# Optimization experiments

Measured on AMD Instinct MI355X. Metric: run time of the kernel, lower is better.

## Reference

```python
import jax, jax.numpy as jnp
import numpy as np

N_HEAD = 16


def setup_inputs() -> dict:
    key = jax.random.key(0)
    ks = jax.random.split(key, 6)
    B, T, H = 4, 2048, 1024
    inp = jax.random.normal(ks[0], (B, T, H), dtype=jnp.float32)
    # padding mask: valid prefix of random length in [T//2, T] per batch row
    lengths = jax.random.randint(ks[1], (B, 1), T // 2, T + 1)
    mask = jnp.arange(T)[None, :] < lengths  # (B, T) bool
    s = 0.02
    w_qkv = jax.random.normal(ks[2], (H, 3 * H), dtype=jnp.float32) * s
    b_qkv = jax.random.normal(ks[3], (3 * H,), dtype=jnp.float32) * s
    w_out = jax.random.normal(ks[4], (H, H), dtype=jnp.float32) * s
    b_out = jax.random.normal(ks[5], (H,), dtype=jnp.float32) * s
    return {"input": inp, "mask": mask, "w_qkv": w_qkv, "b_qkv": b_qkv,
            "w_out": w_out, "b_out": b_out}


def reference(input, mask, w_qkv, b_qkv, w_out, b_out):
    B, T, H = input.shape
    hd = H // N_HEAD
    qkv = input @ w_qkv + b_qkv                       # (B, T, 3H)
    q, k, v = jnp.split(qkv, 3, axis=-1)
    # (B, T, H) -> (B, nh, T, hd)
    q = q.reshape(B, T, N_HEAD, hd).transpose(0, 2, 1, 3)
    k = k.reshape(B, T, N_HEAD, hd).transpose(0, 2, 1, 3)
    v = v.reshape(B, T, N_HEAD, hd).transpose(0, 2, 1, 3)
    scores = jnp.einsum('bhqd,bhkd->bhqk', q, k) / jnp.sqrt(jnp.float32(hd))
    causal = jnp.tril(jnp.ones((T, T), dtype=bool))   # (T, T)
    full_mask = causal[None, None, :, :] & mask[:, None, None, :]  # (B,1,T,T) bcast over heads
    scores = jnp.where(full_mask, scores, -jnp.inf)
    attn = jax.nn.softmax(scores, axis=-1)            # (B, nh, T, T)
    o = jnp.einsum('bhqk,bhkd->bhqd', attn, v)        # (B, nh, T, hd)
    o = o.transpose(0, 2, 1, 3).reshape(B, T, H)
    return o @ w_out + b_out
```

## Files before the change

### kernel.cpp

```cpp
#include <hip/hip_runtime.h>
#include <math.h>

#define B_  4
#define T_  2048
#define H_  1024
#define NH  16
#define HD  64
#define H3  3072

typedef short bf16x8 __attribute__((ext_vector_type(8)));
typedef short bf16x4 __attribute__((ext_vector_type(4)));
typedef float f32x4  __attribute__((ext_vector_type(4)));

#define SC2F 0.18033688011112042f

__device__ __forceinline__ unsigned short f2bf(float f) {
    union { float f; unsigned u; } v; v.f = f;
    unsigned u = v.u;
    unsigned r = (u + 0x7fffu + ((u >> 16) & 1u)) >> 16;
    return (unsigned short)r;
}

__device__ __forceinline__ void gload_lds16(const void* g, void* l) {
    __builtin_amdgcn_global_load_lds(
        (const __attribute__((address_space(1))) unsigned*)g,
        (__attribute__((address_space(3))) unsigned*)l, 16, 0, 0);
}

__device__ __forceinline__ f32x4 mfma_16x16x16_bf16(bf16x4 a, bf16x4 b, f32x4 c) {
#if __has_builtin(__builtin_amdgcn_mfma_f32_16x16x16_bf16)
    return __builtin_amdgcn_mfma_f32_16x16x16_bf16(a, b, c, 0, 0, 0);
#elif __has_builtin(__builtin_amdgcn_mfma_f32_16x16x16bf16_1k)
    return __builtin_amdgcn_mfma_f32_16x16x16bf16_1k(a, b, c, 0, 0, 0);
#else
    f32x4 d;
    asm volatile("v_mfma_f32_16x16x16_bf16 %0, %1, %2, %3"
                 : "=v"(d) : "v"(a), "v"(b), "v"(c));
    return d;
#endif
}

__global__ void lengths_kernel(const void* mask, int* lengths) {
    int b = blockIdx.x;
    int t = threadIdx.x;
    const unsigned* mu = (const unsigned*)mask;
    bool is_byte = (mu[0] == 0x01010101u);
    int cnt = 0;
    if (is_byte) {
        const unsigned char* m8 = (const unsigned char*)mask;
        for (int i = t; i < T_; i += 256) cnt += (m8[b * T_ + i] != 0);
    } else {
        const unsigned* m32 = (const unsigned*)mask;
        for (int i = t; i < T_; i += 256) cnt += (m32[b * T_ + i] != 0);
    }
    __shared__ int red[256];
    red[t] = cnt;
    __syncthreads();
    for (int s = 128; s > 0; s >>= 1) {
        if (t < s) red[t] += red[t + s];
        __syncthreads();
    }
    if (t == 0) lengths[b] = red[0];
}

__global__ void convert_bf16_kernel(const float* __restrict__ x,
                                    unsigned short* __restrict__ y, int n) {
    int i = (blockIdx.x * 256 + threadIdx.x) * 4;
    if (i < n) {
        float4 v = *(const float4*)(x + i);
        ushort4 o;
        o.x = f2bf(v.x); o.y = f2bf(v.y); o.z = f2bf(v.z); o.w = f2bf(v.w);
        *(ushort4*)(y + i) = o;
    }
}

__global__ void transpose_bf16_kernel(const float* __restrict__ in,
                                      unsigned short* __restrict__ out,
                                      int K, int N) {
    __shared__ unsigned short tile[32][33];
    int kb = blockIdx.y * 32, nb = blockIdx.x * 32;
    int tx = threadIdx.x, ty = threadIdx.y;
    for (int i = 0; i < 32; i += 8)
        tile[ty + i][tx] = f2bf(in[(long)(kb + ty + i) * N + nb + tx]);
    __syncthreads();
    for (int i = 0; i < 32; i += 8)
        out[(long)(nb + ty + i) * K + kb + tx] = tile[tx][ty + i];
}

template <bool BF16_OUT, bool KSCALE, bool VSPLIT>
__global__ __launch_bounds__(256) void gemm_kernel(
    const unsigned short* __restrict__ A,
    const unsigned short* __restrict__ Bt,
    const float* __restrict__ bias,
    void* __restrict__ C,
    unsigned short* __restrict__ Vt,
    int M, int N, int K)
{
    __shared__ unsigned short Asm[128][32];
    __shared__ unsigned short Bsm[128][32];

    int tn = blockIdx.x * 128, tm = blockIdx.y * 128;
    int tid = threadIdx.x;
    int wid = tid >> 6, lane = tid & 63, quad = lane >> 4, lr = lane & 15;
    int wm = (wid & 1) * 64, wn = (wid >> 1) * 64;
    int grow = lane >> 2, gcol = (lane & 3) * 8;

    f32x4 acc[4][4] = {};

    for (int k0 = 0; k0 < K; k0 += 32) {
        __syncthreads();
#pragma unroll
        for (int t = 0; t < 2; t++) {
            int ar = wid * 32 + t * 16 + grow;
            gload_lds16(A  + (long)(tm + ar) * K + k0 + gcol, &Asm[wid * 32 + t * 16][0]);
            gload_lds16(Bt + (long)(tn + ar) * K + k0 + gcol, &Bsm[wid * 32 + t * 16][0]);
        }
        __syncthreads();

        bf16x8 af[4], bfv[4];
#pragma unroll
        for (int i = 0; i < 4; i++) af[i]  = *(const bf16x8*)(&Asm[wm + i * 16 + lr][quad * 8]);
#pragma unroll
        for (int j = 0; j < 4; j++) bfv[j] = *(const bf16x8*)(&Bsm[wn + j * 16 + lr][quad * 8]);
#pragma unroll
        for (int i = 0; i < 4; i++)
#pragma unroll
            for (int j = 0; j < 4; j++)
                acc[i][j] = __builtin_amdgcn_mfma_f32_16x16x32_bf16(af[i], bfv[j], acc[i][j], 0, 0, 0);
    }

    if (VSPLIT && tn >= 2 * H_) {
#pragma unroll
        for (int i = 0; i < 4; i++)
#pragma unroll
            for (int j = 0; j < 4; j++) {
                int col = tn + wn + j * 16 + lr;
                float bs = bias[col];
                int feat = col - 2 * H_;
                int tok0 = tm + wm + i * 16 + quad * 4;
                int bb = tok0 >> 11;
                unsigned d0 = (unsigned)f2bf(acc[i][j][0] + bs) |
                              ((unsigned)f2bf(acc[i][j][1] + bs) << 16);
                unsigned d1 = (unsigned)f2bf(acc[i][j][2] + bs) |
                              ((unsigned)f2bf(acc[i][j][3] + bs) << 16);
                unsigned short* dst = Vt + ((long)(bb * 1024 + feat)) * T_ + (tok0 & (T_ - 1));
                *(uint2*)dst = make_uint2(d0, d1);
            }
        return;
    }

#pragma unroll
    for (int i = 0; i < 4; i++)
#pragma unroll
        for (int j = 0; j < 4; j++) {
            int col = tn + wn + j * 16 + lr;
            float bs = bias[col];
            bool ks = KSCALE && (col >= H_) && (col < 2 * H_);
#pragma unroll
            for (int r = 0; r < 4; r++) {
                int row = tm + wm + i * 16 + quad * 4 + r;
                float v = acc[i][j][r] + bs;
                if (ks) v *= SC2F;
                if (BF16_OUT)
                    ((unsigned short*)C)[(long)row * N + col] = f2bf(v);
                else
                    ((float*)C)[(long)row * N + col] = v;
            }
        }
}

__global__ __launch_bounds__(256) void attn_kernel(
    const unsigned short* __restrict__ QKV,
    const unsigned short* __restrict__ Vt,
    const int* __restrict__ lengths,
    unsigned short* __restrict__ O)
{
    int idx = blockIdx.x;
    int bh = idx & 63;
    int pr = idx >> 6;
    int b = bh >> 4, h = bh & 15;
    int len = lengths[b];

    int tid = threadIdx.x;
    int wid = tid >> 6, lane = tid & 63, quad = lane >> 4, lr = lane & 15;

    __shared__ unsigned short Qs[128][72];
    __shared__ unsigned short Kd[2][64][72];
    __shared__ unsigned short Vd[2][64][72];

    const long qkv_base = (long)b * T_ * H3;
    int srow = tid >> 2, scb = (tid & 3) * 16;
    const unsigned short* kbase = QKV + qkv_base + (long)srow * H3 + H_ + h * HD + scb;
    const unsigned short* vbase = Vt + ((long)(bh * 64 + srow)) * T_ + scb;

    for (int pass = 0; pass < 2; pass++) {
        int qt = pass ? pr : (15 - pr);
        int q0 = qt * 128;

        __syncthreads();
        {
            int row = tid >> 1, cb = (tid & 1) * 32;
            const unsigned short* src = QKV + qkv_base + (long)(q0 + row) * H3 + h * HD + cb;
#pragma unroll
            for (int i = 0; i < 4; i++)
                *(float4*)(&Qs[row][cb + i * 8]) = *(const float4*)(src + i * 8);
        }
        {
            float4 k0 = *(const float4*)(kbase);
            float4 k1 = *(const float4*)(kbase + 8);
            float4 v0 = *(const float4*)(vbase);
            float4 v1 = *(const float4*)(vbase + 8);
            *(float4*)(&Kd[0][srow][scb])     = k0;
            *(float4*)(&Kd[0][srow][scb + 8]) = k1;
            *(float4*)(&Vd[0][srow][scb])     = v0;
            *(float4*)(&Vd[0][srow][scb + 8]) = v1;
        }
        __syncthreads();

        bf16x8 qf[2][2];
#pragma unroll
        for (int nq = 0; nq < 2; nq++)
#pragma unroll
            for (int ks = 0; ks < 2; ks++)
                qf[nq][ks] = *(const bf16x8*)(&Qs[wid * 32 + nq * 16 + lr][ks * 32 + quad * 8]);

        float l_i[2] = { 0.f, 0.f };
        f32x4 Oacc[4][2] = {};

        int kmax = min(q0 + 127, len - 1);
        int n_kt = (kmax >> 6) + 1;
        int q_wave_lo = q0 + wid * 32;
        int q_wave_hi = q_wave_lo + 31;
        int myq[2] = { q_wave_lo + lr, q_wave_lo + 16 + lr };

        const unsigned short* kp = kbase + (long)64 * H3;
        const unsigned short* vp = vbase + 64;

        for (int kt = 0; kt < n_kt; kt++) {
            int cur = kt & 1;
            float4 pk0, pk1, pv0, pv1;
            bool pf = (kt + 1 < n_kt);
            if (pf) {
                pk0 = *(const float4*)(kp);
                pk1 = *(const float4*)(kp + 8);
                pv0 = *(const float4*)(vp);
                pv1 = *(const float4*)(vp + 8);
                kp += (long)64 * H3;
                vp += 64;
            }

            int k_lo = kt * 64;
            if (!(k_lo > q_wave_hi || k_lo >= len)) {
                f32x4 Sacc[4][2] = {};
#pragma unroll
                for (int ks = 0; ks < 2; ks++) {
#pragma unroll
                    for (int mt = 0; mt < 4; mt++) {
                        bf16x8 kf = *(const bf16x8*)(&Kd[cur][mt * 16 + lr][ks * 32 + quad * 8]);
                        Sacc[mt][0] = __builtin_amdgcn_mfma_f32_16x16x32_bf16(kf, qf[0][ks], Sacc[mt][0], 0, 0, 0);
                        Sacc[mt][1] = __builtin_amdgcn_mfma_f32_16x16x32_bf16(kf, qf[1][ks], Sacc[mt][1], 0, 0, 0);
                    }
                }

                bool full = (k_lo + 63 <= q_wave_lo) && (k_lo + 63 < len);
                float rs[2] = { 0.f, 0.f };
                unsigned pkk[4][2][2];
#pragma unroll
                for (int mt = 0; mt < 4; mt++)
#pragma unroll
                    for (int nq = 0; nq < 2; nq++) {
                        float p[4];
#pragma unroll
                        for (int r = 0; r < 4; r++) {
                            float s = Sacc[mt][nq][r];
                            if (!full) {
                                int key = k_lo + mt * 16 + quad * 4 + r;
                                bool ok = (key <= myq[nq]) && (key < len);
                                s = ok ? s : -INFINITY;
                            }
                            p[r] = __builtin_amdgcn_exp2f(s);
                            rs[nq] += p[r];
                        }
                        pkk[mt][nq][0] = __builtin_amdgcn_perm(__float_as_uint(p[1]), __float_as_uint(p[0]), 0x07060302);
                        pkk[mt][nq][1] = __builtin_amdgcn_perm(__float_as_uint(p[3]), __float_as_uint(p[2]), 0x07060302);
                    }

#pragma unroll
                for (int nq = 0; nq < 2; nq++) {
                    float v = rs[nq];
                    v += __shfl_xor(v, 16);
                    v += __shfl_xor(v, 32);
                    l_i[nq] += v;
                }

#pragma unroll
                for (int mt = 0; mt < 4; mt++) {
                    union { unsigned u[2]; bf16x4 v; } bu[2];
                    bu[0].u[0] = pkk[mt][0][0]; bu[0].u[1] = pkk[mt][0][1];
                    bu[1].u[0] = pkk[mt][1][0]; bu[1].u[1] = pkk[mt][1][1];
#pragma unroll
                    for (int md = 0; md < 4; md++) {
                        bf16x4 vf = *(const bf16x4*)(&Vd[cur][md * 16 + lr][mt * 16 + quad * 4]);
                        Oacc[md][0] = mfma_16x16x16_bf16(vf, bu[0].v, Oacc[md][0]);
                        Oacc[md][1] = mfma_16x16x16_bf16(vf, bu[1].v, Oacc[md][1]);
                    }
                }
            }

            if (pf) {
                *(float4*)(&Kd[cur ^ 1][srow][scb])     = pk0;
                *(float4*)(&Kd[cur ^ 1][srow][scb + 8]) = pk1;
                *(float4*)(&Vd[cur ^ 1][srow][scb])     = pv0;
                *(float4*)(&Vd[cur ^ 1][srow][scb + 8]) = pv1;
            }
            __syncthreads();
        }

        {
            float inv[2] = { 1.f / l_i[0], 1.f / l_i[1] };
#pragma unroll
            for (int nq = 0; nq < 2; nq++)
#pragma unroll
                for (int md = 0; md < 4; md++)
#pragma unroll
                    for (int rp = 0; rp < 2; rp++) {
                        float e0 = Oacc[md][nq][rp * 2]     * inv[nq];
                        float e1 = Oacc[md][nq][rp * 2 + 1] * inv[nq];
                        unsigned w = __builtin_amdgcn_perm(__float_as_uint(e1), __float_as_uint(e0), 0x07060302);
                        *(unsigned*)(&Qs[wid * 32 + nq * 16 + lr][md * 16 + quad * 4 + rp * 2]) = w;
                    }
            __asm__ volatile("s_waitcnt lgkmcnt(0)" ::: "memory");
            int row = lane >> 1, cb = (lane & 1) * 32;
            long tok = (long)b * T_ + q0 + wid * 32 + row;
#pragma unroll
            for (int i = 0; i < 4; i++) {
                float4 v = *(const float4*)(&Qs[wid * 32 + row][cb + i * 8]);
                *(float4*)(&O[tok * H_ + h * HD + cb + i * 8]) = v;
            }
        }
    }
}

extern "C" void kernel_launch(void* const* d_in, const int* in_sizes, int n_in,
                              void* d_out, int out_size, void* d_ws, size_t ws_size,
                              hipStream_t stream) {
    const float* X    = (const float*)d_in[0];
    const void*  mask = d_in[1];
    const float* Wqkv = (const float*)d_in[2];
    const float* bqkv = (const float*)d_in[3];
    const float* Wout = (const float*)d_in[4];
    const float* bout = (const float*)d_in[5];

    char* ws = (char*)d_ws;
    int* lengths          = (int*)ws;
    unsigned short* WqkvT = (unsigned short*)(ws + 256);
    unsigned short* WoutT = WqkvT + (long)H3 * H_;
    unsigned short* QKV   = WoutT + (long)H_ * H_;
    unsigned short* Xbf   = QKV + (long)B_ * T_ * H3;
    unsigned short* Vt    = Xbf + (long)B_ * T_ * H_;
    unsigned short* Obf   = Xbf;

    const int M = B_ * T_;

    lengths_kernel<<<B_, 256, 0, stream>>>(mask, lengths);
    convert_bf16_kernel<<<(M * H_ / 4 + 255) / 256, 256, 0, stream>>>(X, Xbf, M * H_);
    transpose_bf16_kernel<<<dim3(H3 / 32, H_ / 32), dim3(32, 8), 0, stream>>>(Wqkv, WqkvT, H_, H3);
    transpose_bf16_kernel<<<dim3(H_ / 32, H_ / 32), dim3(32, 8), 0, stream>>>(Wout, WoutT, H_, H_);
    gemm_kernel<true, true, true><<<dim3(H3 / 128, M / 128), 256, 0, stream>>>(
        Xbf, WqkvT, bqkv, QKV, Vt, M, H3, H_);
    attn_kernel<<<B_ * NH * 8, 256, 0, stream>>>(QKV, Vt, lengths, Obf);
    gemm_kernel<false, false, false><<<dim3(H_ / 128, M / 128), 256, 0, stream>>>(
        Obf, WoutT, bout, d_out, nullptr, M, H_, H_);
}
```

Measured before the change: 300.0 us.

## Use 32x32 MFMA with swizzled LDS in GEMM, one q-tile per attention block

```diff
diff --git a/kernel.cpp b/kernel.cpp
--- a/kernel.cpp
+++ b/kernel.cpp
@@ -11,6 +11,7 @@
 typedef short bf16x8 __attribute__((ext_vector_type(8)));
 typedef short bf16x4 __attribute__((ext_vector_type(4)));
 typedef float f32x4  __attribute__((ext_vector_type(4)));
+typedef float f32x16 __attribute__((ext_vector_type(16)));
 
 #define SC2F 0.18033688011112042f
 
@@ -74,11 +75,18 @@
     }
 }
 
-__global__ void transpose_bf16_kernel(const float* __restrict__ in,
-                                      unsigned short* __restrict__ out,
-                                      int K, int N) {
+__global__ void transpose2_kernel(const float* __restrict__ Wqkv,
+                                  unsigned short* __restrict__ WqkvT,
+                                  const float* __restrict__ Wout,
+                                  unsigned short* __restrict__ WoutT) {
     __shared__ unsigned short tile[32][33];
-    int kb = blockIdx.y * 32, nb = blockIdx.x * 32;
+    const int K = H_;
+    const float* in;
+    unsigned short* out;
+    int N, nb;
+    if (blockIdx.x < 96) { in = Wqkv; out = WqkvT; N = H3; nb = blockIdx.x * 32; }
+    else                 { in = Wout; out = WoutT; N = H_; nb = (blockIdx.x - 96) * 32; }
+    int kb = blockIdx.y * 32;
     int tx = threadIdx.x, ty = threadIdx.y;
     for (int i = 0; i < 32; i += 8)
         tile[ty + i][tx] = f2bf(in[(long)(kb + ty + i) * N + nb + tx]);
@@ -101,11 +109,14 @@
 
     int tn = blockIdx.x * 128, tm = blockIdx.y * 128;
     int tid = threadIdx.x;
-    int wid = tid >> 6, lane = tid & 63, quad = lane >> 4, lr = lane & 15;
+    int wid = tid >> 6, lane = tid & 63;
+    int l31 = lane & 31, lh = lane >> 5;
     int wm = (wid & 1) * 64, wn = (wid >> 1) * 64;
-    int grow = lane >> 2, gcol = (lane & 3) * 8;
-
-    f32x4 acc[4][4] = {};
+    int grow = lane >> 2;
+    int gcol = (((lane & 3) ^ (grow & 3) ^ ((grow >> 2) & 3))) * 8;
+    int rkey = (l31 & 3) ^ ((l31 >> 2) & 3);
+
+    f32x16 acc[2][2] = {};
 
     for (int k0 = 0; k0 < K; k0 += 32) {
         __syncthreads();
@@ -117,50 +128,60 @@
         }
         __syncthreads();
 
-        bf16x8 af[4], bfv[4];
-#pragma unroll
-        for (int i = 0; i < 4; i++) af[i]  = *(const bf16x8*)(&Asm[wm + i * 16 + lr][quad * 8]);
-#pragma unroll
-        for (int j = 0; j < 4; j++) bfv[j] = *(const bf16x8*)(&Bsm[wn + j * 16 + lr][quad * 8]);
-#pragma unroll
-        for (int i = 0; i < 4; i++)
-#pragma unroll
-            for (int j = 0; j < 4; j++)
-                acc[i][j] = __builtin_amdgcn_mfma_f32_16x16x32_bf16(af[i], bfv[j], acc[i][j], 0, 0, 0);
+        bf16x8 af[2][2], bfv[2][2];
+#pragma unroll
+        for (int ks = 0; ks < 2; ks++) {
+            int pc = ((2 * ks + lh) ^ rkey) * 8;
+            af[ks][0]  = *(const bf16x8*)(&Asm[wm + l31][pc]);
+            af[ks][1]  = *(const bf16x8*)(&Asm[wm + 32 + l31][pc]);
+            bfv[ks][0] = *(const bf16x8*)(&Bsm[wn + l31][pc]);
+            bfv[ks][1] = *(const bf16x8*)(&Bsm[wn + 32 + l31][pc]);
+        }
+#pragma unroll
+        for (int ks = 0; ks < 2; ks++)
+#pragma unroll
+            for (int i = 0; i < 2; i++)
+#pragma unroll
+                for (int j = 0; j < 2; j++)
+                    acc[i][j] = __builtin_amdgcn_mfma_f32_32x32x16_bf16(
+                        af[ks][i], bfv[ks][j], acc[i][j], 0, 0, 0);
     }
 
     if (VSPLIT && tn >= 2 * H_) {
 #pragma unroll
-        for (int i = 0; i < 4; i++)
-#pragma unroll
-            for (int j = 0; j < 4; j++) {
-                int col = tn + wn + j * 16 + lr;
+        for (int i = 0; i < 2; i++)
+#pragma unroll
+            for (int j = 0; j < 2; j++) {
+                int col = tn + wn + j * 32 + l31;
                 float bs = bias[col];
                 int feat = col - 2 * H_;
-                int tok0 = tm + wm + i * 16 + quad * 4;
-                int bb = tok0 >> 11;
-                unsigned d0 = (unsigned)f2bf(acc[i][j][0] + bs) |
-                              ((unsigned)f2bf(acc[i][j][1] + bs) << 16);
-                unsigned d1 = (unsigned)f2bf(acc[i][j][2] + bs) |
-                              ((unsigned)f2bf(acc[i][j][3] + bs) << 16);
-                unsigned short* dst = Vt + ((long)(bb * 1024 + feat)) * T_ + (tok0 & (T_ - 1));
-                *(uint2*)dst = make_uint2(d0, d1);
+#pragma unroll
+                for (int rg = 0; rg < 4; rg++) {
+                    int tok0 = tm + wm + i * 32 + rg * 8 + lh * 4;
+                    int bb = tok0 >> 11;
+                    unsigned d0 = (unsigned)f2bf(acc[i][j][rg * 4 + 0] + bs) |
+                                  ((unsigned)f2bf(acc[i][j][rg * 4 + 1] + bs) << 16);
+                    unsigned d1 = (unsigned)f2bf(acc[i][j][rg * 4 + 2] + bs) |
+                                  ((unsigned)f2bf(acc[i][j][rg * 4 + 3] + bs) << 16);
+                    unsigned short* dst = Vt + ((long)(bb * 1024 + feat)) * T_ + (tok0 & (T_ - 1));
+                    *(uint2*)dst = make_uint2(d0, d1);
+                }
             }
         return;
     }
 
 #pragma unroll
-    for (int i = 0; i < 4; i++)
-#pragma unroll
-        for (int j = 0; j < 4; j++) {
-            int col = tn + wn + j * 16 + lr;
+    for (int i = 0; i < 2; i++)
+#pragma unroll
+        for (int j = 0; j < 2; j++) {
+            int col = tn + wn + j * 32 + l31;
             float bs = bias[col];
-            bool ks = KSCALE && (col >= H_) && (col < 2 * H_);
-#pragma unroll
-            for (int r = 0; r < 4; r++) {
-                int row = tm + wm + i * 16 + quad * 4 + r;
+            bool ks_ = KSCALE && (col >= H_) && (col < 2 * H_);
+#pragma unroll
+            for (int r = 0; r < 16; r++) {
+                int row = tm + wm + i * 32 + (r & 3) + 8 * (r >> 2) + 4 * lh;
                 float v = acc[i][j][r] + bs;
-                if (ks) v *= SC2F;
+                if (ks_) v *= SC2F;
                 if (BF16_OUT)
                     ((unsigned short*)C)[(long)row * N + col] = f2bf(v);
                 else
@@ -177,166 +198,158 @@
 {
     int idx = blockIdx.x;
     int bh = idx & 63;
-    int pr = idx >> 6;
+    int qt = 15 - (idx >> 6);
     int b = bh >> 4, h = bh & 15;
     int len = lengths[b];
+    int q0 = qt * 128;
 
     int tid = threadIdx.x;
     int wid = tid >> 6, lane = tid & 63, quad = lane >> 4, lr = lane & 15;
 
-    __shared__ unsigned short Qs[128][72];
-    __shared__ unsigned short Kd[2][64][72];
-    __shared__ unsigned short Vd[2][64][72];
+    __shared__ __align__(16) unsigned short SH[18432];
+    unsigned short (*Kd)[64][72] = (unsigned short (*)[64][72])(&SH[0]);
+    unsigned short (*Vd)[64][72] = (unsigned short (*)[64][72])(&SH[9216]);
 
     const long qkv_base = (long)b * T_ * H3;
+
+    bf16x8 qf[2][2];
+#pragma unroll
+    for (int nq = 0; nq < 2; nq++)
+#pragma unroll
+        for (int ks = 0; ks < 2; ks++)
+            qf[nq][ks] = *(const bf16x8*)(QKV + qkv_base +
+                (long)(q0 + wid * 32 + nq * 16 + lr) * H3 + h * HD + ks * 32 + quad * 8);
+
     int srow = tid >> 2, scb = (tid & 3) * 16;
     const unsigned short* kbase = QKV + qkv_base + (long)srow * H3 + H_ + h * HD + scb;
     const unsigned short* vbase = Vt + ((long)(bh * 64 + srow)) * T_ + scb;
 
-    for (int pass = 0; pass < 2; pass++) {
-        int qt = pass ? pr : (15 - pr);
-        int q0 = qt * 128;
-
+    {
+        float4 k0 = *(const float4*)(kbase);
+        float4 k1 = *(const float4*)(kbase + 8);
+        float4 v0 = *(const float4*)(vbase);
+        float4 v1 = *(const float4*)(vbase + 8);
+        *(float4*)(&Kd[0][srow][scb])     = k0;
+        *(float4*)(&Kd[0][srow][scb + 8]) = k1;
+        *(float4*)(&Vd[0][srow][scb])     = v0;
+        *(float4*)(&Vd[0][srow][scb + 8]) = v1;
+    }
+    __syncthreads();
+
+    float l_i[2] = { 0.f, 0.f };
+    f32x4 Oacc[4][2] = {};
+
+    int kmax = min(q0 + 127, len - 1);
+    int n_kt = (kmax >> 6) + 1;
+    int q_wave_lo = q0 + wid * 32;
+    int q_wave_hi = q_wave_lo + 31;
+    int myq[2] = { q_wave_lo + lr, q_wave_lo + 16 + lr };
+
+    const unsigned short* kp = kbase + (long)64 * H3;
+    const unsigned short* vp = vbase + 64;
+
+    for (int kt = 0; kt < n_kt; kt++) {
+        int cur = kt & 1;
+        float4 pk0, pk1, pv0, pv1;
+        bool pf = (kt + 1 < n_kt);
+        if (pf) {
+            pk0 = *(const float4*)(kp);
+            pk1 = *(const float4*)(kp + 8);
+            pv0 = *(const float4*)(vp);
+            pv1 = *(const float4*)(vp + 8);
+            kp += (long)64 * H3;
+            vp += 64;
+        }
+
+        int k_lo = kt * 64;
+        if (!(k_lo > q_wave_hi || k_lo >= len)) {
+            f32x4 Sacc[4][2] = {};
+#pragma unroll
+            for (int ks = 0; ks < 2; ks++) {
+#pragma unroll
+                for (int mt = 0; mt < 4; mt++) {
+                    bf16x8 kf = *(const bf16x8*)(&Kd[cur][mt * 16 + lr][ks * 32 + quad * 8]);
+                    Sacc[mt][0] = __builtin_amdgcn_mfma_f32_16x16x32_bf16(kf, qf[0][ks], Sacc[mt][0], 0, 0, 0);
+                    Sacc[mt][1] = __builtin_amdgcn_mfma_f32_16x16x32_bf16(kf, qf[1][ks], Sacc[mt][1], 0, 0, 0);
+                }
+            }
+
+            bool full = (k_lo + 63 <= q_wave_lo) && (k_lo + 63 < len);
+            float rs[2] = { 0.f, 0.f };
+            unsigned pkk[4][2][2];
+#pragma unroll
+            for (int mt = 0; mt < 4; mt++)
+#pragma unroll
+                for (int nq = 0; nq < 2; nq++) {
+                    float p[4];
+#pragma unroll
+                    for (int r = 0; r < 4; r++) {
+                        float s = Sacc[mt][nq][r];
+                        if (!full) {
+                            int key = k_lo + mt * 16 + quad * 4 + r;
+                            bool ok = (key <= myq[nq]) && (key < len);
+                            s = ok ? s : -INFINITY;
+                        }
+                        p[r] = __builtin_amdgcn_exp2f(s);
+                        rs[nq] += p[r];
+                    }
+                    pkk[mt][nq][0] = __builtin_amdgcn_perm(__float_as_uint(p[1]), __float_as_uint(p[0]), 0x07060302);
+                    pkk[mt][nq][1] = __builtin_amdgcn_perm(__float_as_uint(p[3]), __float_as_uint(p[2]), 0x07060302);
+                }
+
+#pragma unroll
+            for (int nq = 0; nq < 2; nq++) {
+                float v = rs[nq];
+                v += __shfl_xor(v, 16);
+                v += __shfl_xor(v, 32);
+                l_i[nq] += v;
+            }
+
+#pragma unroll
+            for (int mt = 0; mt < 4; mt++) {
+                union { unsigned u[2]; bf16x4 v; } bu[2];
+                bu[0].u[0] = pkk[mt][0][0]; bu[0].u[1] = pkk[mt][0][1];
+                bu[1].u[0] = pkk[mt][1][0]; bu[1].u[1] = pkk[mt][1][1];
+#pragma unroll
+                for (int md = 0; md < 4; md++) {
+                    bf16x4 vf = *(const bf16x4*)(&Vd[cur][md * 16 + lr][mt * 16 + quad * 4]);
+                    Oacc[md][0] = mfma_16x16x16_bf16(vf, bu[0].v, Oacc[md][0]);
+                    Oacc[md][1] = mfma_16x16x16_bf16(vf, bu[1].v, Oacc[md][1]);
+                }
+            }
+        }
+
+        if (pf) {
+            *(float4*)(&Kd[cur ^ 1][srow][scb])     = pk0;
+            *(float4*)(&Kd[cur ^ 1][srow][scb + 8]) = pk1;
+            *(float4*)(&Vd[cur ^ 1][srow][scb])     = pv0;
+            *(float4*)(&Vd[cur ^ 1][srow][scb + 8]) = pv1;
+        }
         __syncthreads();
-        {
-            int row = tid >> 1, cb = (tid & 1) * 32;
-            const unsigned short* src = QKV + qkv_base + (long)(q0 + row) * H3 + h * HD + cb;
-#pragma unroll
-            for (int i = 0; i < 4; i++)
-                *(float4*)(&Qs[row][cb + i * 8]) = *(const float4*)(src + i * 8);
-        }
-        {
-            float4 k0 = *(const float4*)(kbase);
-            float4 k1 = *(const float4*)(kbase + 8);
-            float4 v0 = *(const float4*)(vbase);
-            float4 v1 = *(const float4*)(vbase + 8);
-            *(float4*)(&Kd[0][srow][scb])     = k0;
-            *(float4*)(&Kd[0][srow][scb + 8]) = k1;
-            *(float4*)(&Vd[0][srow][scb])     = v0;
-            *(float4*)(&Vd[0][srow][scb + 8]) = v1;
-        }
-        __syncthreads();
-
-        bf16x8 qf[2][2];
+    }
+
+    __syncthreads();
+    {
+        unsigned short (*Es)[68] = (unsigned short (*)[68])(&SH[0]);
+        float inv[2] = { 1.f / l_i[0], 1.f / l_i[1] };
 #pragma unroll
         for (int nq = 0; nq < 2; nq++)
 #pragma unroll
-            for (int ks = 0; ks < 2; ks++)
-                qf[nq][ks] = *(const bf16x8*)(&Qs[wid * 32 + nq * 16 + lr][ks * 32 + quad * 8]);
-
-        float l_i[2] = { 0.f, 0.f };
-        f32x4 Oacc[4][2] = {};
-
-        int kmax = min(q0 + 127, len - 1);
-        int n_kt = (kmax >> 6) + 1;
-        int q_wave_lo = q0 + wid * 32;
-        int q_wave_hi = q_wave_lo + 31;
-        int myq[2] = { q_wave_lo + lr, q_wave_lo + 16 + lr };
-
-        const unsigned short* kp = kbase + (long)64 * H3;
-        const unsigned short* vp = vbase + 64;
-
-        for (int kt = 0; kt < n_kt; kt++) {
-            int cur = kt & 1;
-            float4 pk0, pk1, pv0, pv1;
-            bool pf = (kt + 1 < n_kt);
-            if (pf) {
-                pk0 = *(const float4*)(kp);
-                pk1 = *(const float4*)(kp + 8);
-                pv0 = *(const float4*)(vp);
-                pv1 = *(const float4*)(vp + 8);
-                kp += (long)64 * H3;
-                vp += 64;
-            }
-
-            int k_lo = kt * 64;
-            if (!(k_lo > q_wave_hi || k_lo >= len)) {
-                f32x4 Sacc[4][2] = {};
-#pragma unroll
-                for (int ks = 0; ks < 2; ks++) {
-#pragma unroll
-                    for (int mt = 0; mt < 4; mt++) {
-                        bf16x8 kf = *(const bf16x8*)(&Kd[cur][mt * 16 + lr][ks * 32 + quad * 8]);
-                        Sacc[mt][0] = __builtin_amdgcn_mfma_f32_16x16x32_bf16(kf, qf[0][ks], Sacc[mt][0], 0, 0, 0);
-                        Sacc[mt][1] = __builtin_amdgcn_mfma_f32_16x16x32_bf16(kf, qf[1][ks], Sacc[mt][1], 0, 0, 0);
-                    }
-                }
-
-                bool full = (k_lo + 63 <= q_wave_lo) && (k_lo + 63 < len);
-                float rs[2] = { 0.f, 0.f };
-                unsigned pkk[4][2][2];
-#pragma unroll
-                for (int mt = 0; mt < 4; mt++)
-#pragma unroll
-                    for (int nq = 0; nq < 2; nq++) {
-                        float p[4];
-#pragma unroll
-                        for (int r = 0; r < 4; r++) {
-                            float s = Sacc[mt][nq][r];
-                            if (!full) {
-                                int key = k_lo + mt * 16 + quad * 4 + r;
-                                bool ok = (key <= myq[nq]) && (key < len);
-                                s = ok ? s : -INFINITY;
-                            }
-                            p[r] = __builtin_amdgcn_exp2f(s);
-                            rs[nq] += p[r];
-                        }
-                        pkk[mt][nq][0] = __builtin_amdgcn_perm(__float_as_uint(p[1]), __float_as_uint(p[0]), 0x07060302);
-                        pkk[mt][nq][1] = __builtin_amdgcn_perm(__float_as_uint(p[3]), __float_as_uint(p[2]), 0x07060302);
-                    }
-
-#pragma unroll
-                for (int nq = 0; nq < 2; nq++) {
-                    float v = rs[nq];
-                    v += __shfl_xor(v, 16);
-                    v += __shfl_xor(v, 32);
-                    l_i[nq] += v;
-                }
-
-#pragma unroll
-                for (int mt = 0; mt < 4; mt++) {
-                    union { unsigned u[2]; bf16x4 v; } bu[2];
-                    bu[0].u[0] = pkk[mt][0][0]; bu[0].u[1] = pkk[mt][0][1];
-                    bu[1].u[0] = pkk[mt][1][0]; bu[1].u[1] = pkk[mt][1][1];
-#pragma unroll
-                    for (int md = 0; md < 4; md++) {
-                        bf16x4 vf = *(const bf16x4*)(&Vd[cur][md * 16 + lr][mt * 16 + quad * 4]);
-                        Oacc[md][0] = mfma_16x16x16_bf16(vf, bu[0].v, Oacc[md][0]);
-                        Oacc[md][1] = mfma_16x16x16_bf16(vf, bu[1].v, Oacc[md][1]);
-                    }
-                }
-            }
-
-            if (pf) {
-                *(float4*)(&Kd[cur ^ 1][srow][scb])     = pk0;
-                *(float4*)(&Kd[cur ^ 1][srow][scb + 8]) = pk1;
-                *(float4*)(&Vd[cur ^ 1][srow][scb])     = pv0;
-                *(float4*)(&Vd[cur ^ 1][srow][scb + 8]) = pv1;
-            }
-            __syncthreads();
-        }
-
-        {
-            float inv[2] = { 1.f / l_i[0], 1.f / l_i[1] };
-#pragma unroll
-            for (int nq = 0; nq < 2; nq++)
-#pragma unroll
-                for (int md = 0; md < 4; md++)
-#pragma unroll
-                    for (int rp = 0; rp < 2; rp++) {
-                        float e0 = Oacc[md][nq][rp * 2]     * inv[nq];
-                        float e1 = Oacc[md][nq][rp * 2 + 1] * inv[nq];
-                        unsigned w = __builtin_amdgcn_perm(__float_as_uint(e1), __float_as_uint(e0), 0x07060302);
-                        *(unsigned*)(&Qs[wid * 32 + nq * 16 + lr][md * 16 + quad * 4 + rp * 2]) = w;
-                    }
-            __asm__ volatile("s_waitcnt lgkmcnt(0)" ::: "memory");
-            int row = lane >> 1, cb = (lane & 1) * 32;
-            long tok = (long)b * T_ + q0 + wid * 32 + row;
-#pragma unroll
-            for (int i = 0; i < 4; i++) {
-                float4 v = *(const float4*)(&Qs[wid * 32 + row][cb + i * 8]);
-                *(float4*)(&O[tok * H_ + h * HD + cb + i * 8]) = v;
-            }
+            for (int md = 0; md < 4; md++)
+#pragma unroll
+                for (int rp = 0; rp < 2; rp++) {
+                    float e0 = Oacc[md][nq][rp * 2]     * inv[nq];
+                    float e1 = Oacc[md][nq][rp * 2 + 1] * inv[nq];
+                    unsigned w = __builtin_amdgcn_perm(__float_as_uint(e1), __float_as_uint(e0), 0x07060302);
+                    *(unsigned*)(&Es[wid * 32 + nq * 16 + lr][md * 16 + quad * 4 + rp * 2]) = w;
+                }
+        __asm__ volatile("s_waitcnt lgkmcnt(0)" ::: "memory");
+        int row = lane >> 1, cb = (lane & 1) * 32;
+        long tok = (long)b * T_ + q0 + wid * 32 + row;
+#pragma unroll
+        for (int i = 0; i < 4; i++) {
+            float4 v = *(const float4*)(&Es[wid * 32 + row][cb + i * 8]);
+            *(float4*)(&O[tok * H_ + h * HD + cb + i * 8]) = v;
         }
     }
 }
@@ -364,11 +377,10 @@
 
     lengths_kernel<<<B_, 256, 0, stream>>>(mask, lengths);
     convert_bf16_kernel<<<(M * H_ / 4 + 255) / 256, 256, 0, stream>>>(X, Xbf, M * H_);
-    transpose_bf16_kernel<<<dim3(H3 / 32, H_ / 32), dim3(32, 8), 0, stream>>>(Wqkv, WqkvT, H_, H3);
-    transpose_bf16_kernel<<<dim3(H_ / 32, H_ / 32), dim3(32, 8), 0, stream>>>(Wout, WoutT, H_, H_);
+    transpose2_kernel<<<dim3(128, H_ / 32), dim3(32, 8), 0, stream>>>(Wqkv, WqkvT, Wout, WoutT);
     gemm_kernel<true, true, true><<<dim3(H3 / 128, M / 128), 256, 0, stream>>>(
         Xbf, WqkvT, bqkv, QKV, Vt, M, H3, H_);
-    attn_kernel<<<B_ * NH * 8, 256, 0, stream>>>(QKV, Vt, lengths, Obf);
+    attn_kernel<<<B_ * NH * (T_ / 128), 256, 0, stream>>>(QKV, Vt, lengths, Obf);
     gemm_kernel<false, false, false><<<dim3(H_ / 128, M / 128), 256, 0, stream>>>(
         Obf, WoutT, bout, d_out, nullptr, M, H_, H_);
 }
```

Result: faster. 287.6 us (-4.1%).
